# Performance work log

Hardware: AMD Instinct MI355X
Metric: run time of the kernel (lower is better)

Reference implementation:

```python
import jax, jax.numpy as jnp
import numpy as np

B, C, T, E = 8, 64, 128, 256
TYPE_NUM, NF = 40, 128
KS = (5, 4, 3)
NEG = -1e10


def setup_inputs() -> dict:
    key = jax.random.key(0)
    ks = jax.random.split(key, 10)
    s = 0.02
    return {
        "query": jax.random.normal(ks[0], (C, E), jnp.float32),
        "context": jax.random.normal(ks[1], (B, T, E), jnp.float32),
        "mask": jax.random.randint(ks[2], (B, T), 0, 2, jnp.int32),
        "W_hidden": jax.random.normal(ks[3], (4 * E, 4 * E), jnp.float32) * s,
        "b_hidden": jnp.zeros((4 * E,), jnp.float32),
        "W_v": jax.random.normal(ks[4], (1, 4 * E), jnp.float32) * s,
        "b_v": jnp.zeros((1,), jnp.float32),
        "W_lin": jax.random.normal(ks[5], (E, 4 * E), jnp.float32) * s,
        "b_lin": jnp.zeros((E,), jnp.float32),
        "conv_w0": jax.random.normal(ks[6], (NF, E, KS[0]), jnp.float32) * s,
        "conv_b0": jnp.zeros((NF,), jnp.float32),
        "conv_w1": jax.random.normal(ks[7], (NF, E, KS[1]), jnp.float32) * s,
        "conv_b1": jnp.zeros((NF,), jnp.float32),
        "conv_w2": jax.random.normal(ks[8], (NF, E, KS[2]), jnp.float32) * s,
        "conv_b2": jnp.zeros((NF,), jnp.float32),
        "W_cnn": jax.random.normal(ks[9], (TYPE_NUM, NF * 3), jnp.float32) * s,
        "b_cnn": jnp.zeros((TYPE_NUM,), jnp.float32),
    }


def _pair_feat(a, b):
    # [.., e] x2 -> [.., 4e]: [a, b, |a-b|, a*b]
    return jnp.concatenate([a, b, jnp.abs(a - b), a * b], axis=-1)


def _conv1d(x, w, b):
    # x: [b, e, c], w: [f, e, k] (torch Conv1d layout) -> [b, f, c-k+1]
    y = jax.lax.conv_general_dilated(
        x, w, window_strides=(1,), padding="VALID",
        dimension_numbers=("NCH", "OIH", "NCH"))
    return y + b[None, :, None]


def reference(query, context, mask, W_hidden, b_hidden, W_v, b_v,
              W_lin, b_lin, conv_w0, conv_b0, conv_w1, conv_b1,
              conv_w2, conv_b2, W_cnn, b_cnn):
    b, t, e = context.shape
    c = query.shape[0]
    q_ = jnp.broadcast_to(query[None, :, None, :], (b, c, t, e))
    ctx_ = jnp.broadcast_to(context[:, None, :, :], (b, c, t, e))
    feat = _pair_feat(q_, ctx_)                                 # [b,c,t,4e]
    h = jnp.tanh(feat @ W_hidden.T + b_hidden)                  # [b,c,t,4e]
    scores = (h @ W_v.T + b_v)[..., 0]                          # [b,c,t]
    scores = jnp.where((mask < 1)[:, None, :], NEG, scores)
    attn = jax.nn.softmax(scores, axis=-1)                      # [b,c,t]
    g = jnp.einsum("bct,bte->bce", attn, context)               # [b,c,e]
    q2 = jnp.broadcast_to(query[None], (b, c, e))
    h2 = jnp.tanh(_pair_feat(q2, g) @ W_hidden.T + b_hidden)    # [b,c,4e]
    x = h2 @ W_lin.T + b_lin                                    # [b,c,e]
    xT = jnp.transpose(x, (0, 2, 1))                            # [b,e,c]
    pooled = []
    for w, bb in ((conv_w0, conv_b0), (conv_w1, conv_b1), (conv_w2, conv_b2)):
        y = jax.nn.relu(_conv1d(xT, w, bb))                     # [b,f,c-k+1]
        pooled.append(jnp.max(y, axis=2))                       # [b,f]
    cnn = jnp.concatenate(pooled, axis=1)                       # [b,3f]
    return cnn @ W_cnn.T + b_cnn                                # [b,type_num]
```

## Files before the change

kernel.cpp:

```cpp
#include <hip/hip_runtime.h>
#include <math.h>


typedef __bf16 bf16x8 __attribute__((ext_vector_type(8)));
typedef float  f32x4  __attribute__((ext_vector_type(4)));

__device__ __forceinline__ float ftanh(float v) {
    float t = __expf(2.f * v);
    return 1.f - 2.f * __builtin_amdgcn_rcpf(t + 1.f);
}

__device__ __forceinline__ void gld_lds16(const __bf16* g, __bf16* l) {
    __builtin_amdgcn_global_load_lds(
        (const __attribute__((address_space(1))) void*)g,
        (__attribute__((address_space(3))) void*)l, 16, 0, 0);
}

__device__ __forceinline__ bf16x8 cvt8(float4 f0, float4 f1) {
    bf16x8 u;
    u[0] = (__bf16)f0.x; u[1] = (__bf16)f0.y; u[2] = (__bf16)f0.z; u[3] = (__bf16)f0.w;
    u[4] = (__bf16)f1.x; u[5] = (__bf16)f1.y; u[6] = (__bf16)f1.z; u[7] = (__bf16)f1.w;
    return u;
}

__global__ __launch_bounds__(256) void cvt_kernel(
    const float* __restrict__ Wh, const float* __restrict__ Wl,
    const float* __restrict__ ctx,
    const float* __restrict__ cw0, const float* __restrict__ cw1,
    const float* __restrict__ cw2,
    const float* __restrict__ q, const float* __restrict__ bh,
    float* __restrict__ Apre, float* __restrict__ x, float* __restrict__ Bpre,
    __bf16* __restrict__ Whbf, __bf16* __restrict__ Whbf_t,
    __bf16* __restrict__ Wlbf,
    float* __restrict__ wt0, float* __restrict__ wt1,
    float* __restrict__ wt2, float* __restrict__ gsc,
    float* __restrict__ cnn)
{
    __shared__ __align__(16) char smem[18432];
    const int bx = blockIdx.x;
    const int tid = threadIdx.x;

    if (bx < 16) {
        float (*As)[68] = reinterpret_cast<float(*)[68]>(smem);
        float (*Bs)[68] = reinterpret_cast<float(*)[68]>(smem + 4352);
        const int n0 = bx * 64;
        const int tm = tid >> 4, tn = tid & 15;
        const int lr = tid >> 2;
        const int lc = (tid & 3) * 4;

        float acc[4][4];
#pragma unroll
        for (int i = 0; i < 4; ++i)
#pragma unroll
            for (int j = 0; j < 4; ++j) acc[i][j] = 0.f;

        for (int k0 = 0; k0 < 256; k0 += 16) {
            float4 av = *reinterpret_cast<const float4*>(q + (size_t)lr * 256 + k0 + lc);
            float4 bv = *reinterpret_cast<const float4*>(Wh + (size_t)(n0 + lr) * 1024 + k0 + lc);
            As[lc + 0][lr] = av.x; As[lc + 1][lr] = av.y; As[lc + 2][lr] = av.z; As[lc + 3][lr] = av.w;
            Bs[lc + 0][lr] = bv.x; Bs[lc + 1][lr] = bv.y; Bs[lc + 2][lr] = bv.z; Bs[lc + 3][lr] = bv.w;
            __syncthreads();
#pragma unroll
            for (int kk = 0; kk < 16; ++kk) {
                float4 a = *reinterpret_cast<const float4*>(&As[kk][tm * 4]);
                float4 b = *reinterpret_cast<const float4*>(&Bs[kk][tn * 4]);
                float ar[4] = {a.x, a.y, a.z, a.w};
                float br[4] = {b.x, b.y, b.z, b.w};
#pragma unroll
                for (int i = 0; i < 4; ++i)
#pragma unroll
                    for (int j = 0; j < 4; ++j) acc[i][j] += ar[i] * br[j];
            }
            __syncthreads();
        }

#pragma unroll
        for (int i = 0; i < 4; ++i) {
            int m = tm * 4 + i;
            float vals[4];
#pragma unroll
            for (int j = 0; j < 4; ++j) vals[j] = acc[i][j] + bh[n0 + tn * 4 + j];
            float4 o; o.x = vals[0]; o.y = vals[1]; o.z = vals[2]; o.w = vals[3];
            *reinterpret_cast<float4*>(Apre + (size_t)m * 1024 + n0 + tn * 4) = o;
        }
        return;
    }

    if (bx < 272) {
        __bf16* As = reinterpret_cast<__bf16*>(smem);
        __bf16* Bs = As + 64 * 72;
        const int bid = bx - 16;
        const int m0 = (bid >> 4) * 64, n0 = (bid & 15) * 64;
        const int wave = tid >> 6, lane = tid & 63;
        const int w0 = wave >> 1, w1 = wave & 1;
        const int l15 = lane & 15, quad = lane >> 4;

        f32x4 acc[2][2];
#pragma unroll
        for (int mi = 0; mi < 2; ++mi)
#pragma unroll
            for (int ni = 0; ni < 2; ++ni) acc[mi][ni] = (f32x4){0.f, 0.f, 0.f, 0.f};

        for (int k0 = 0; k0 < 256; k0 += 64) {
            __syncthreads();
#pragma unroll
            for (int it = 0; it < 2; ++it) {
                int idx = tid + it * 256;
                int row = idx >> 3, kgi = idx & 7;
                const float* sa = ctx + (size_t)(m0 + row) * 256 + k0 + kgi * 8;
                float4 a0 = *reinterpret_cast<const float4*>(sa);
                float4 a1 = *reinterpret_cast<const float4*>(sa + 4);
                *reinterpret_cast<bf16x8*>(&As[row * 72 + kgi * 8]) = cvt8(a0, a1);
                const float* sb = Wh + (size_t)(n0 + row) * 1024 + 256 + k0 + kgi * 8;
                float4 b0 = *reinterpret_cast<const float4*>(sb);
                float4 b1 = *reinterpret_cast<const float4*>(sb + 4);
                *reinterpret_cast<bf16x8*>(&Bs[row * 72 + kgi * 8]) = cvt8(b0, b1);
            }
            __syncthreads();
#pragma unroll
            for (int ks = 0; ks < 2; ++ks) {
                bf16x8 a[2], bb[2];
#pragma unroll
                for (int mi = 0; mi < 2; ++mi)
                    a[mi] = *reinterpret_cast<const bf16x8*>(
                        &As[(w0 * 32 + mi * 16 + l15) * 72 + ks * 32 + quad * 8]);
#pragma unroll
                for (int ni = 0; ni < 2; ++ni)
                    bb[ni] = *reinterpret_cast<const bf16x8*>(
                        &Bs[(w1 * 32 + ni * 16 + l15) * 72 + ks * 32 + quad * 8]);
#pragma unroll
                for (int mi = 0; mi < 2; ++mi)
#pragma unroll
                    for (int ni = 0; ni < 2; ++ni)
                        acc[mi][ni] = __builtin_amdgcn_mfma_f32_16x16x32_bf16(
                            a[mi], bb[ni], acc[mi][ni], 0, 0, 0);
            }
        }

#pragma unroll
        for (int mi = 0; mi < 2; ++mi)
#pragma unroll
            for (int ni = 0; ni < 2; ++ni) {
                int col = n0 + w1 * 32 + ni * 16 + l15;
#pragma unroll
                for (int r = 0; r < 4; ++r) {
                    int row = m0 + w0 * 32 + mi * 16 + quad * 4 + r;
                    Bpre[(size_t)row * 1024 + col] = acc[mi][ni][r];
                }
            }
        return;
    }

    int idx = (bx - 272) * 256 + tid;
    if (idx < 131072) {
        const float* s = Wh + (size_t)idx * 8;
        float4 f0 = *reinterpret_cast<const float4*>(s);
        float4 f1 = *reinterpret_cast<const float4*>(s + 4);
        *reinterpret_cast<bf16x8*>(Whbf + (size_t)idx * 8) = cvt8(f0, f1);
        return;
    }
    if (idx < 196608) {
        int di = idx - 131072;
        int ng = di >> 13, kc = (di >> 10) & 7;
        int row = (di >> 3) & 127, kgp = di & 7;
        int kg = kgp ^ (row & 7);
        const float* s = Wh + (size_t)(ng * 128 + row) * 1024 + 512 + kc * 64 + kg * 8;
        float4 f0 = *reinterpret_cast<const float4*>(s);
        float4 f1 = *reinterpret_cast<const float4*>(s + 4);
        *reinterpret_cast<bf16x8*>(Whbf_t + (size_t)di * 8) = cvt8(f0, f1);
        return;
    }
    if (idx < 229376) {
        int di = idx - 196608;
        const float* s = Wl + (size_t)di * 8;
        float4 f0 = *reinterpret_cast<const float4*>(s);
        float4 f1 = *reinterpret_cast<const float4*>(s + 4);
        *reinterpret_cast<bf16x8*>(Wlbf + (size_t)di * 8) = cvt8(f0, f1);
        return;
    }
    if (idx < 393216) {
        int j = idx - 229376; int f = j & 127, rest = j >> 7;
        int i = rest % 5, e = rest / 5;
        wt0[j] = cw0[(size_t)(f * 256 + e) * 5 + i]; return;
    }
    if (idx < 524288) {
        int j = idx - 393216; int f = j & 127, rest = j >> 7;
        int i = rest & 3, e = rest >> 2;
        wt1[j] = cw1[(size_t)(f * 256 + e) * 4 + i]; return;
    }
    if (idx < 622592) {
        int j = idx - 524288; int f = j & 127, rest = j >> 7;
        int i = rest % 3, e = rest / 3;
        wt2[j] = cw2[(size_t)(f * 256 + e) * 3 + i]; return;
    }
    if (idx < 638976) {
        int di = idx - 622592;
        reinterpret_cast<float4*>(gsc)[di] = (float4){0.f, 0.f, 0.f, 0.f};
        return;
    }
    if (idx < 642048) { cnn[idx - 638976] = 0.f; return; }
    if (idx < 674816) {
        int di = idx - 642048;
        reinterpret_cast<float4*>(x)[di] = (float4){0.f, 0.f, 0.f, 0.f};
    }
}

__global__ __launch_bounds__(512, 4) void attn_mfma_kernel(
    const float* __restrict__ q,
    const float* __restrict__ ctx,
    const __bf16* __restrict__ Whbf_t,
    const float* __restrict__ Wv,
    const float* __restrict__ Apre,
    const float* __restrict__ Bpre,
    float* __restrict__ gsc)
{
    __shared__ __bf16 Us[256 * 64];
    __shared__ __bf16 Ws[128 * 64];
    __shared__ float qc[512];
    __shared__ float sc[256];

    const int tid = threadIdx.x;
    const int cpair = blockIdx.x >> 3, ng = blockIdx.x & 7;
    const int b = cpair >> 5, c0 = (cpair & 31) * 2;
    const int wave = tid >> 6, lane = tid & 63;
    const int w1 = wave & 1, w0 = wave >> 1;
    const int m0 = w0 * 64;
    const int l15 = lane & 15, quad = lane >> 4;
    const int swz = l15 & 7;
    const int kg = tid & 7;

    qc[tid] = q[(size_t)(c0 + (tid >> 8)) * 256 + (tid & 255)];
    if (tid < 256) sc[tid] = 0.f;
    __syncthreads();

    f32x4 acc[4][4];
#pragma unroll
    for (int mi = 0; mi < 4; ++mi)
#pragma unroll
        for (int ni = 0; ni < 4; ++ni) acc[mi][ni] = (f32x4){0.f, 0.f, 0.f, 0.f};

    for (int kc = 0; kc < 8; ++kc) {
        const bool isabs = (kc < 4);
        const int e0 = (kc & 3) * 64;
        const int eb = e0 + kg * 8;
        float qA[8], qB[8];
#pragma unroll
        for (int i = 0; i < 8; ++i) { qA[i] = qc[eb + i]; qB[i] = qc[256 + eb + i]; }
        bf16x8 u0[2], u1[2];
#pragma unroll
        for (int it = 0; it < 2; ++it) {
            const int trow = it * 64 + (tid >> 3);
            const float* cp = ctx + (size_t)(b * 128 + trow) * 256 + eb;
            float4 cl0 = *reinterpret_cast<const float4*>(cp);
            float4 cl1 = *reinterpret_cast<const float4*>(cp + 4);
            float cv[8] = {cl0.x, cl0.y, cl0.z, cl0.w, cl1.x, cl1.y, cl1.z, cl1.w};
#pragma unroll
            for (int i = 0; i < 8; ++i) {
                u0[it][i] = (__bf16)(isabs ? fabsf(qA[i] - cv[i]) : qA[i] * cv[i]);
                u1[it][i] = (__bf16)(isabs ? fabsf(qB[i] - cv[i]) : qB[i] * cv[i]);
            }
        }
        __syncthreads();
        const __bf16* wtile = Whbf_t + (size_t)(ng * 8 + kc) * 8192;
#pragma unroll
        for (int it = 0; it < 2; ++it) {
            int gidx = wave * 128 + it * 64;
            gld_lds16(wtile + (size_t)(gidx + lane) * 8, &Ws[gidx * 8]);
        }
#pragma unroll
        for (int it = 0; it < 2; ++it) {
            const int trow = it * 64 + (tid >> 3);
            const int off = (kg ^ (trow & 7)) * 8;
            *reinterpret_cast<bf16x8*>(&Us[trow * 64 + off]) = u0[it];
            *reinterpret_cast<bf16x8*>(&Us[(trow + 128) * 64 + off]) = u1[it];
        }
        __syncthreads();
#pragma unroll
        for (int ks = 0; ks < 2; ++ks) {
            const int c8 = (((ks * 4 + quad) ^ swz)) * 8;
            bf16x8 a[4], bfr[4];
#pragma unroll
            for (int mi = 0; mi < 4; ++mi)
                a[mi] = *reinterpret_cast<const bf16x8*>(
                    &Us[(m0 + mi * 16 + l15) * 64 + c8]);
#pragma unroll
            for (int ni = 0; ni < 4; ++ni)
                bfr[ni] = *reinterpret_cast<const bf16x8*>(
                    &Ws[(w1 * 64 + ni * 16 + l15) * 64 + c8]);
#pragma unroll
            for (int mi = 0; mi < 4; ++mi)
#pragma unroll
                for (int ni = 0; ni < 4; ++ni)
                    acc[mi][ni] = __builtin_amdgcn_mfma_f32_16x16x32_bf16(
                        a[mi], bfr[ni], acc[mi][ni], 0, 0, 0);
        }
    }

    const int jcol = ng * 128 + w1 * 64 + l15;
    const int c = c0 + (w0 >> 1);
    float av[4], wv[4];
#pragma unroll
    for (int ni = 0; ni < 4; ++ni) {
        av[ni] = Apre[(size_t)c * 1024 + jcol + ni * 16];
        wv[ni] = Wv[jcol + ni * 16];
    }
#pragma unroll
    for (int mi = 0; mi < 4; ++mi) {
        const int tb = (w0 & 1) * 64 + mi * 16 + quad * 4;
        float p[4];
#pragma unroll
        for (int r = 0; r < 4; ++r) {
            const float* bp = Bpre + (size_t)(b * 128 + tb + r) * 1024 + jcol;
            float s = 0.f;
#pragma unroll
            for (int ni = 0; ni < 4; ++ni)
                s += ftanh(acc[mi][ni][r] + av[ni] + bp[ni * 16]) * wv[ni];
            p[r] = s;
        }
#pragma unroll
        for (int off = 1; off < 16; off <<= 1)
#pragma unroll
            for (int r = 0; r < 4; ++r) p[r] += __shfl_xor(p[r], off, 16);
        if (l15 == 0) {
#pragma unroll
            for (int r = 0; r < 4; ++r)
                atomicAdd(&sc[(w0 >> 1) * 128 + tb + r], p[r]);
        }
    }
    __syncthreads();

    if (tid < 256) atomicAdd(&gsc[(size_t)(b * 64 + c0) * 128 + tid], sc[tid]);
}

__global__ __launch_bounds__(256) void attn_tail_kernel(
    const float* __restrict__ ctx, const int* __restrict__ mask,
    const float* __restrict__ bv, const float* __restrict__ gsc,
    const float* __restrict__ q, __bf16* __restrict__ feat2,
    float* __restrict__ h2pre)
{
    __shared__ float sc[128];
    __shared__ float red;
    const int tid = threadIdx.x;
    const int bc = blockIdx.x, b = bc >> 6, c = bc & 63;

    reinterpret_cast<float4*>(h2pre)[(size_t)bc * 256 + tid] =
        (float4){0.f, 0.f, 0.f, 0.f};

    if (tid < 128) {
        float s = gsc[(size_t)bc * 128 + tid] + bv[0];
        if (mask[b * 128 + tid] < 1) s = -1e10f;
        sc[tid] = s;
    }
    __syncthreads();
    if (tid < 64) {
        float m = fmaxf(sc[tid], sc[tid + 64]);
        for (int off = 32; off; off >>= 1) m = fmaxf(m, __shfl_xor(m, off, 64));
        if (tid == 0) red = m;
    }
    __syncthreads();
    const float mx = red;
    if (tid < 128) sc[tid] = __expf(sc[tid] - mx);
    __syncthreads();
    if (tid < 64) {
        float s = sc[tid] + sc[tid + 64];
        for (int off = 32; off; off >>= 1) s += __shfl_xor(s, off, 64);
        if (tid == 0) red = s;
    }
    __syncthreads();
    const float inv = 1.f / red;

    float gv = 0.f;
#pragma unroll 16
    for (int t = 0; t < 128; ++t) gv += sc[t] * ctx[(size_t)(b * 128 + t) * 256 + tid];
    gv *= inv;
    const float qv = q[(size_t)c * 256 + tid];
    __bf16* o = feat2 + (size_t)bc * 768 + tid;
    o[0]   = (__bf16)gv;
    o[256] = (__bf16)fabsf(qv - gv);
    o[512] = (__bf16)(qv * gv);
}

template <int ACT, int OUTBF, int BMODE, int ATOMIC, int ATANH>
__global__ __launch_bounds__(256) void mfma_gemm_kernel(
    const void* __restrict__ A, int lda,
    const __bf16* __restrict__ B, int ldb,
    const float* __restrict__ bias, void* __restrict__ Cout,
    int K, int ldc)
{
    __shared__ __bf16 As[64 * 72];
    __shared__ __bf16 Bs[64 * 72];
    const int tid = threadIdx.x;
    const int wave = tid >> 6, lane = tid & 63;
    const int w0 = wave >> 1, w1 = wave & 1;
    const int l15 = lane & 15, quad = lane >> 4;
    const int m0 = blockIdx.y * 64, n0 = blockIdx.x * 64;

    int kbeg = 0, kend = K;
    if (ATOMIC) {
        int kchunk = K / gridDim.z;
        kbeg = blockIdx.z * kchunk;
        kend = kbeg + kchunk;
    }

    f32x4 acc[2][2];
#pragma unroll
    for (int mi = 0; mi < 2; ++mi)
#pragma unroll
        for (int ni = 0; ni < 2; ++ni) acc[mi][ni] = (f32x4){0.f, 0.f, 0.f, 0.f};

    for (int k0 = kbeg; k0 < kend; k0 += 64) {
        __syncthreads();
#pragma unroll
        for (int it = 0; it < 2; ++it) {
            int idx = tid + it * 256;
            int row = idx >> 3, kgi = idx & 7;
            if (ATANH) {
                const float* sa = (const float*)A + (size_t)(m0 + row) * lda + k0 + kgi * 8;
                float4 a0 = *reinterpret_cast<const float4*>(sa);
                float4 a1 = *reinterpret_cast<const float4*>(sa + 4);
                bf16x8 u;
                u[0] = (__bf16)ftanh(a0.x); u[1] = (__bf16)ftanh(a0.y);
                u[2] = (__bf16)ftanh(a0.z); u[3] = (__bf16)ftanh(a0.w);
                u[4] = (__bf16)ftanh(a1.x); u[5] = (__bf16)ftanh(a1.y);
                u[6] = (__bf16)ftanh(a1.z); u[7] = (__bf16)ftanh(a1.w);
                *reinterpret_cast<bf16x8*>(&As[row * 72 + kgi * 8]) = u;
            } else {
                int4 va = *reinterpret_cast<const int4*>(
                    (const __bf16*)A + (size_t)(m0 + row) * lda + k0 + kgi * 8);
                *reinterpret_cast<int4*>(&As[row * 72 + kgi * 8]) = va;
            }
            int4 vb = *reinterpret_cast<const int4*>(B + (size_t)(n0 + row) * ldb + k0 + kgi * 8);
            *reinterpret_cast<int4*>(&Bs[row * 72 + kgi * 8]) = vb;
        }
        __syncthreads();
#pragma unroll
        for (int ks = 0; ks < 2; ++ks) {
            bf16x8 a[2], bb[2];
#pragma unroll
            for (int mi = 0; mi < 2; ++mi)
                a[mi] = *reinterpret_cast<const bf16x8*>(
                    &As[(w0 * 32 + mi * 16 + l15) * 72 + ks * 32 + quad * 8]);
#pragma unroll
            for (int ni = 0; ni < 2; ++ni)
                bb[ni] = *reinterpret_cast<const bf16x8*>(
                    &Bs[(w1 * 32 + ni * 16 + l15) * 72 + ks * 32 + quad * 8]);
#pragma unroll
            for (int mi = 0; mi < 2; ++mi)
#pragma unroll
                for (int ni = 0; ni < 2; ++ni)
                    acc[mi][ni] = __builtin_amdgcn_mfma_f32_16x16x32_bf16(
                        a[mi], bb[ni], acc[mi][ni], 0, 0, 0);
        }
    }

#pragma unroll
    for (int mi = 0; mi < 2; ++mi)
#pragma unroll
        for (int ni = 0; ni < 2; ++ni) {
            int col = n0 + w1 * 32 + ni * 16 + l15;
#pragma unroll
            for (int r = 0; r < 4; ++r) {
                int row = m0 + w0 * 32 + mi * 16 + quad * 4 + r;
                float bsv = (BMODE == 0) ? bias[col]
                          : (BMODE == 1) ? bias[(row & 63) * 1024 + col] : 0.f;
                if (ATOMIC) {
                    float v = acc[mi][ni][r] + (blockIdx.z == 0 ? bsv : 0.f);
                    atomicAdd((float*)Cout + (size_t)row * ldc + col, v);
                } else {
                    float v = acc[mi][ni][r] + bsv;
                    if (ACT) v = ftanh(v);
                    if (OUTBF) ((__bf16*)Cout)[(size_t)row * ldc + col] = (__bf16)v;
                    else       ((float*)Cout)[(size_t)row * ldc + col] = v;
                }
            }
        }
}

template <int KW>
__device__ __forceinline__ void conv_body(
    const float* __restrict__ x, const float* __restrict__ wt,
    float* __restrict__ part, int b, int chunk, int bi_part, int pbase, float* xs)
{
    const int tid = threadIdx.x;
    const int f = tid & 127, esub = tid >> 7;
    const int e0 = chunk * 64;

#pragma unroll
    for (int it = 0; it < 16; ++it) {
        int idx = tid + it * 256;
        int e = idx & 63, p = idx >> 6;
        xs[e * 72 + p] = x[(size_t)(b * 64 + p) * 256 + e0 + e];
    }
    __syncthreads();

    float acc[32];
#pragma unroll
    for (int p = 0; p < 32; ++p) acc[p] = 0.f;

    for (int ei = 0; ei < 32; ++ei) {
        const int eL = esub * 32 + ei;
        float wreg[KW];
#pragma unroll
        for (int i = 0; i < KW; ++i)
            wreg[i] = wt[(size_t)((e0 + eL) * KW + i) * 128 + f];
        float xv[36];
#pragma unroll
        for (int k4 = 0; k4 < 9; ++k4) {
            float4 v = *reinterpret_cast<const float4*>(&xs[eL * 72 + pbase + k4 * 4]);
            xv[k4 * 4 + 0] = v.x; xv[k4 * 4 + 1] = v.y;
            xv[k4 * 4 + 2] = v.z; xv[k4 * 4 + 3] = v.w;
        }
#pragma unroll
        for (int i = 0; i < KW; ++i)
#pragma unroll
            for (int p = 0; p < 32; ++p)
                acc[p] = fmaf(wreg[i], xv[p + i], acc[p]);
    }

    float* op = part + ((size_t)(bi_part * 2 + esub)) * 8192 + f;
#pragma unroll
    for (int p = 0; p < 32; ++p) op[(pbase + p) * 128] = acc[p];
}

__global__ __launch_bounds__(256) void conv_partial_kernel(
    const float* __restrict__ x,
    const float* __restrict__ wt0, const float* __restrict__ wt1,
    const float* __restrict__ wt2, float* __restrict__ part)
{
    __shared__ float xs[64 * 72];
    const int bi = blockIdx.x;
    const int kw = bi >> 6, b = (bi >> 3) & 7, chunk = (bi >> 1) & 3;
    const int pbase = (bi & 1) * 32;
    const int bi_part = kw * 32 + b * 4 + chunk;
    if (kw == 0)      conv_body<5>(x, wt0, part, b, chunk, bi_part, pbase, xs);
    else if (kw == 1) conv_body<4>(x, wt1, part, b, chunk, bi_part, pbase, xs);
    else              conv_body<3>(x, wt2, part, b, chunk, bi_part, pbase, xs);
}

__global__ __launch_bounds__(128) void reduce_pool_kernel(
    const float* __restrict__ part,
    const float* __restrict__ b0, const float* __restrict__ b1,
    const float* __restrict__ b2, float* __restrict__ cnn)
{
    const int bi = blockIdx.x;
    const int kw = bi >> 6, b = (bi >> 3) & 7, pc = bi & 7;
    const int f = threadIdx.x;
    const int KW = 5 - kw, P = 64 - KW + 1;
    const float bias = (kw == 0 ? b0 : kw == 1 ? b1 : b2)[f];
    float mx = 0.f;
#pragma unroll
    for (int pl = 0; pl < 8; ++pl) {
        int p = pc * 8 + pl;
        if (p < P) {
            float s = 0.f;
#pragma unroll
            for (int c4 = 0; c4 < 4; ++c4)
#pragma unroll
                for (int es = 0; es < 2; ++es)
                    s += part[((size_t)((kw * 32 + b * 4 + c4) * 2 + es)) * 8192 + p * 128 + f];
            s += bias;
            mx = fmaxf(mx, s);
        }
    }
    if (mx > 0.f)
        atomicMax((int*)(cnn + b * 384 + kw * 128 + f), __float_as_int(mx));
}

__global__ void final_kernel(const float* __restrict__ cnn, const float* __restrict__ Wc,
                             const float* __restrict__ bc, float* __restrict__ out)
{
    int o = threadIdx.x;
    if (o >= 320) return;
    int b = o / 40, t = o - b * 40;
    float s = bc[t];
    for (int i = 0; i < 384; ++i) s += cnn[b * 384 + i] * Wc[t * 384 + i];
    out[o] = s;
}

extern "C" void kernel_launch(void* const* d_in, const int* in_sizes, int n_in,
                              void* d_out, int out_size, void* d_ws, size_t ws_size,
                              hipStream_t stream)
{
    (void)in_sizes; (void)n_in; (void)out_size; (void)ws_size;
    const float* q    = (const float*)d_in[0];
    const float* ctx  = (const float*)d_in[1];
    const int*   mask = (const int*)d_in[2];
    const float* Wh   = (const float*)d_in[3];
    const float* bh   = (const float*)d_in[4];
    const float* Wv   = (const float*)d_in[5];
    const float* bv   = (const float*)d_in[6];
    const float* Wl   = (const float*)d_in[7];
    const float* bl   = (const float*)d_in[8];
    const float* cw0  = (const float*)d_in[9];
    const float* cb0  = (const float*)d_in[10];
    const float* cw1  = (const float*)d_in[11];
    const float* cb1  = (const float*)d_in[12];
    const float* cw2  = (const float*)d_in[13];
    const float* cb2  = (const float*)d_in[14];
    const float* Wc   = (const float*)d_in[15];
    const float* bc   = (const float*)d_in[16];

    float* ws   = (float*)d_ws;
    float* Apre = ws;
    float* g    = Apre + 65536;
    float* x    = g + 131072;
    float* cnn  = x + 131072;
    float* part = cnn + 3072;
    float* wt0  = part + 1572864;
    float* wt1  = wt0 + 163840;
    float* wt2  = wt1 + 131072;
    __bf16* bfb    = (__bf16*)(wt2 + 98304);
    __bf16* Whbf   = bfb;
    __bf16* Wlbf   = bfb + 1048576;
    __bf16* feat2b = bfb + 1310720;
    float*  gsc    = (float*)(bfb + 2228224);
    __bf16* Whbf_t = (__bf16*)part;
    float*  Bpre   = (float*)(Whbf_t + 524288);
    float*  h2pre  = Bpre;

    dim3 blk(256);
    cvt_kernel<<<2908, blk, 0, stream>>>(Wh, Wl, ctx, cw0, cw1, cw2, q, bh,
                                         Apre, x, Bpre,
                                         Whbf, Whbf_t, Wlbf, wt0, wt1, wt2,
                                         gsc, cnn);
    attn_mfma_kernel<<<2048, dim3(512), 0, stream>>>(q, ctx, Whbf_t, Wv, Apre, Bpre, gsc);
    attn_tail_kernel<<<512, blk, 0, stream>>>(ctx, mask, bv, gsc, q, feat2b, h2pre);
    mfma_gemm_kernel<0, 0, 1, 1, 0><<<dim3(16, 8, 2), blk, 0, stream>>>(
        feat2b, 768, Whbf + 256, 1024, Apre, h2pre, 768, 1024);
    mfma_gemm_kernel<0, 0, 0, 1, 1><<<dim3(4, 8, 4), blk, 0, stream>>>(
        h2pre, 1024, Wlbf, 1024, bl, x, 1024, 256);
    conv_partial_kernel<<<192, blk, 0, stream>>>(x, wt0, wt1, wt2, part);
    reduce_pool_kernel<<<192, dim3(128), 0, stream>>>(part, cb0, cb1, cb2, cnn);
    final_kernel<<<1, 320, 0, stream>>>(cnn, Wc, bc, (float*)d_out);
}
```

Baseline: 273.1 us.

## Build feature tile once per (b,c) block and loop over all output column groups

The attention MFMA kernel now gives each block a single (batch, query) pair. It builds the full 128x512 bf16 pair-feature operand in LDS once and then iterates over all 8 column groups of W_hidden, where before it recomputed the features per column group across 2048 blocks. Scores are written directly instead of with global atomics. In exchange each block uses about 144KB of LDS, so occupancy drops, and the grid shrinks to 512 blocks.

```diff
diff --git a/kernel.cpp b/kernel.cpp
--- a/kernel.cpp
+++ b/kernel.cpp
@@ -205,7 +205,7 @@
     }
 }
 
-__global__ __launch_bounds__(512, 4) void attn_mfma_kernel(
+__global__ __launch_bounds__(512, 2) void attn_mfma_kernel(
     const float* __restrict__ q,
     const float* __restrict__ ctx,
     const __bf16* __restrict__ Whbf_t,
@@ -214,122 +214,119 @@
     const float* __restrict__ Bpre,
     float* __restrict__ gsc)
 {
-    __shared__ __bf16 Us[256 * 64];
+    __shared__ __bf16 Us[8 * 128 * 64];
     __shared__ __bf16 Ws[128 * 64];
-    __shared__ float qc[512];
-    __shared__ float sc[256];
+    __shared__ float qc[256];
+    __shared__ float sc[128];
 
     const int tid = threadIdx.x;
-    const int cpair = blockIdx.x >> 3, ng = blockIdx.x & 7;
-    const int b = cpair >> 5, c0 = (cpair & 31) * 2;
+    const int bc = blockIdx.x;
+    const int b = bc >> 6, c = bc & 63;
     const int wave = tid >> 6, lane = tid & 63;
-    const int w1 = wave & 1, w0 = wave >> 1;
-    const int m0 = w0 * 64;
+    const int wm = wave >> 2, wn = wave & 3;
+    const int m0 = wm * 64;
     const int l15 = lane & 15, quad = lane >> 4;
     const int swz = l15 & 7;
     const int kg = tid & 7;
-
-    qc[tid] = q[(size_t)(c0 + (tid >> 8)) * 256 + (tid & 255)];
-    if (tid < 256) sc[tid] = 0.f;
+    const int trw = tid >> 3;
+
+    if (tid < 256) qc[tid] = q[(size_t)c * 256 + tid];
+    if (tid < 128) sc[tid] = 0.f;
     __syncthreads();
-
-    f32x4 acc[4][4];
-#pragma unroll
-    for (int mi = 0; mi < 4; ++mi)
-#pragma unroll
-        for (int ni = 0; ni < 4; ++ni) acc[mi][ni] = (f32x4){0.f, 0.f, 0.f, 0.f};
 
     for (int kc = 0; kc < 8; ++kc) {
         const bool isabs = (kc < 4);
-        const int e0 = (kc & 3) * 64;
-        const int eb = e0 + kg * 8;
-        float qA[8], qB[8];
-#pragma unroll
-        for (int i = 0; i < 8; ++i) { qA[i] = qc[eb + i]; qB[i] = qc[256 + eb + i]; }
-        bf16x8 u0[2], u1[2];
+        const int eb = (kc & 3) * 64 + kg * 8;
+        float qv8[8];
+#pragma unroll
+        for (int i = 0; i < 8; ++i) qv8[i] = qc[eb + i];
 #pragma unroll
         for (int it = 0; it < 2; ++it) {
-            const int trow = it * 64 + (tid >> 3);
+            const int trow = it * 64 + trw;
             const float* cp = ctx + (size_t)(b * 128 + trow) * 256 + eb;
             float4 cl0 = *reinterpret_cast<const float4*>(cp);
             float4 cl1 = *reinterpret_cast<const float4*>(cp + 4);
             float cv[8] = {cl0.x, cl0.y, cl0.z, cl0.w, cl1.x, cl1.y, cl1.z, cl1.w};
-#pragma unroll
-            for (int i = 0; i < 8; ++i) {
-                u0[it][i] = (__bf16)(isabs ? fabsf(qA[i] - cv[i]) : qA[i] * cv[i]);
-                u1[it][i] = (__bf16)(isabs ? fabsf(qB[i] - cv[i]) : qB[i] * cv[i]);
-            }
-        }
-        __syncthreads();
-        const __bf16* wtile = Whbf_t + (size_t)(ng * 8 + kc) * 8192;
-#pragma unroll
-        for (int it = 0; it < 2; ++it) {
-            int gidx = wave * 128 + it * 64;
-            gld_lds16(wtile + (size_t)(gidx + lane) * 8, &Ws[gidx * 8]);
-        }
-#pragma unroll
-        for (int it = 0; it < 2; ++it) {
-            const int trow = it * 64 + (tid >> 3);
-            const int off = (kg ^ (trow & 7)) * 8;
-            *reinterpret_cast<bf16x8*>(&Us[trow * 64 + off]) = u0[it];
-            *reinterpret_cast<bf16x8*>(&Us[(trow + 128) * 64 + off]) = u1[it];
-        }
-        __syncthreads();
-#pragma unroll
-        for (int ks = 0; ks < 2; ++ks) {
-            const int c8 = (((ks * 4 + quad) ^ swz)) * 8;
-            bf16x8 a[4], bfr[4];
-#pragma unroll
-            for (int mi = 0; mi < 4; ++mi)
-                a[mi] = *reinterpret_cast<const bf16x8*>(
-                    &Us[(m0 + mi * 16 + l15) * 64 + c8]);
-#pragma unroll
-            for (int ni = 0; ni < 4; ++ni)
-                bfr[ni] = *reinterpret_cast<const bf16x8*>(
-                    &Ws[(w1 * 64 + ni * 16 + l15) * 64 + c8]);
-#pragma unroll
-            for (int mi = 0; mi < 4; ++mi)
-#pragma unroll
-                for (int ni = 0; ni < 4; ++ni)
-                    acc[mi][ni] = __builtin_amdgcn_mfma_f32_16x16x32_bf16(
-                        a[mi], bfr[ni], acc[mi][ni], 0, 0, 0);
-        }
-    }
-
-    const int jcol = ng * 128 + w1 * 64 + l15;
-    const int c = c0 + (w0 >> 1);
-    float av[4], wv[4];
-#pragma unroll
-    for (int ni = 0; ni < 4; ++ni) {
-        av[ni] = Apre[(size_t)c * 1024 + jcol + ni * 16];
-        wv[ni] = Wv[jcol + ni * 16];
-    }
-#pragma unroll
-    for (int mi = 0; mi < 4; ++mi) {
-        const int tb = (w0 & 1) * 64 + mi * 16 + quad * 4;
-        float p[4];
-#pragma unroll
-        for (int r = 0; r < 4; ++r) {
-            const float* bp = Bpre + (size_t)(b * 128 + tb + r) * 1024 + jcol;
-            float s = 0.f;
-#pragma unroll
-            for (int ni = 0; ni < 4; ++ni)
-                s += ftanh(acc[mi][ni][r] + av[ni] + bp[ni * 16]) * wv[ni];
-            p[r] = s;
-        }
-#pragma unroll
-        for (int off = 1; off < 16; off <<= 1)
-#pragma unroll
-            for (int r = 0; r < 4; ++r) p[r] += __shfl_xor(p[r], off, 16);
-        if (l15 == 0) {
-#pragma unroll
-            for (int r = 0; r < 4; ++r)
-                atomicAdd(&sc[(w0 >> 1) * 128 + tb + r], p[r]);
+            bf16x8 u;
+#pragma unroll
+            for (int i = 0; i < 8; ++i)
+                u[i] = (__bf16)(isabs ? fabsf(qv8[i] - cv[i]) : qv8[i] * cv[i]);
+            *reinterpret_cast<bf16x8*>(
+                &Us[kc * 8192 + trow * 64 + (kg ^ (trow & 7)) * 8]) = u;
+        }
+    }
+
+    for (int ng = 0; ng < 8; ++ng) {
+        f32x4 acc[4][2];
+#pragma unroll
+        for (int mi = 0; mi < 4; ++mi)
+#pragma unroll
+            for (int ni = 0; ni < 2; ++ni) acc[mi][ni] = (f32x4){0.f, 0.f, 0.f, 0.f};
+
+        for (int kc = 0; kc < 8; ++kc) {
+            __syncthreads();
+            const __bf16* wtile = Whbf_t + (size_t)(ng * 8 + kc) * 8192;
+#pragma unroll
+            for (int it = 0; it < 2; ++it) {
+                int gidx = wave * 128 + it * 64;
+                gld_lds16(wtile + (size_t)(gidx + lane) * 8, &Ws[gidx * 8]);
+            }
+            __syncthreads();
+#pragma unroll
+            for (int ks = 0; ks < 2; ++ks) {
+                const int c8 = (((ks * 4 + quad) ^ swz)) * 8;
+                bf16x8 a[4], bfr[2];
+#pragma unroll
+                for (int mi = 0; mi < 4; ++mi)
+                    a[mi] = *reinterpret_cast<const bf16x8*>(
+                        &Us[kc * 8192 + (m0 + mi * 16 + l15) * 64 + c8]);
+#pragma unroll
+                for (int ni = 0; ni < 2; ++ni)
+                    bfr[ni] = *reinterpret_cast<const bf16x8*>(
+                        &Ws[(wn * 32 + ni * 16 + l15) * 64 + c8]);
+#pragma unroll
+                for (int mi = 0; mi < 4; ++mi)
+#pragma unroll
+                    for (int ni = 0; ni < 2; ++ni)
+                        acc[mi][ni] = __builtin_amdgcn_mfma_f32_16x16x32_bf16(
+                            a[mi], bfr[ni], acc[mi][ni], 0, 0, 0);
+            }
+        }
+
+        const int jcol = ng * 128 + wn * 32 + l15;
+        float av[2], wv[2];
+#pragma unroll
+        for (int ni = 0; ni < 2; ++ni) {
+            av[ni] = Apre[(size_t)c * 1024 + jcol + ni * 16];
+            wv[ni] = Wv[jcol + ni * 16];
+        }
+#pragma unroll
+        for (int mi = 0; mi < 4; ++mi) {
+            const int tb = m0 + mi * 16 + quad * 4;
+            float p[4];
+#pragma unroll
+            for (int r = 0; r < 4; ++r) {
+                const float* bp = Bpre + (size_t)(b * 128 + tb + r) * 1024 + jcol;
+                float s = 0.f;
+#pragma unroll
+                for (int ni = 0; ni < 2; ++ni)
+                    s += ftanh(acc[mi][ni][r] + av[ni] + bp[ni * 16]) * wv[ni];
+                p[r] = s;
+            }
+#pragma unroll
+            for (int off = 1; off < 16; off <<= 1)
+#pragma unroll
+                for (int r = 0; r < 4; ++r) p[r] += __shfl_xor(p[r], off, 16);
+            if (l15 == 0) {
+#pragma unroll
+                for (int r = 0; r < 4; ++r)
+                    atomicAdd(&sc[tb + r], p[r]);
+            }
         }
     }
     __syncthreads();
 
-    if (tid < 256) atomicAdd(&gsc[(size_t)(b * 64 + c0) * 128 + tid], sc[tid]);
+    if (tid < 128) gsc[(size_t)bc * 128 + tid] = sc[tid];
 }
 
 __global__ __launch_bounds__(256) void attn_tail_kernel(
@@ -623,7 +620,7 @@
                                          Apre, x, Bpre,
                                          Whbf, Whbf_t, Wlbf, wt0, wt1, wt2,
                                          gsc, cnn);
-    attn_mfma_kernel<<<2048, dim3(512), 0, stream>>>(q, ctx, Whbf_t, Wv, Apre, Bpre, gsc);
+    attn_mfma_kernel<<<512, dim3(512), 0, stream>>>(q, ctx, Whbf_t, Wv, Apre, Bpre, gsc);
     attn_tail_kernel<<<512, blk, 0, stream>>>(ctx, mask, bv, gsc, q, feat2b, h2pre);
     mfma_gemm_kernel<0, 0, 1, 1, 0><<<dim3(16, 8, 2), blk, 0, stream>>>(
         feat2b, 768, Whbf + 256, 1024, Apre, h2pre, 768, 1024);
```

Measured after the change: 309.9 us. 1.13x slower.

## Precompute swizzled bf16 pair features in workspace for attention MFMA kernel

Applied to the files above, without the earlier changes.

Adds extra blocks to the conversion kernel that materialise the |q-ctx| and q*ctx pair features in bf16 for every (b,c,t), in a pre-swizzled tile layout written to a large workspace region. A new attention kernel then streams both operand tiles straight into LDS with async global-to-LDS loads, instead of computing features from q and ctx on the fly. This moves the feature arithmetic and bf16 conversion out of the MFMA loop at the cost of writing and re-reading about 64 MB of intermediate data. The new path is taken only when the workspace is large enough; otherwise the old kernel runs.

```diff
diff --git a/kernel.cpp b/kernel.cpp
--- a/kernel.cpp
+++ b/kernel.cpp
@@ -34,11 +34,43 @@
     __bf16* __restrict__ Wlbf,
     float* __restrict__ wt0, float* __restrict__ wt1,
     float* __restrict__ wt2, float* __restrict__ gsc,
-    float* __restrict__ cnn)
+    float* __restrict__ cnn, __bf16* __restrict__ Ubf)
 {
     __shared__ __align__(16) char smem[18432];
     const int bx = blockIdx.x;
     const int tid = threadIdx.x;
+
+    if (bx >= 2908) {
+        int idx2 = (bx - 2908) * 256 + tid;
+        int bc = idx2 >> 10;
+        int rem = idx2 & 1023;
+        int trow = rem >> 3, kg = rem & 7;
+        int b = bc >> 6, c = bc & 63;
+        int gs = kg ^ (trow & 7);
+#pragma unroll
+        for (int ec = 0; ec < 4; ++ec) {
+            int eb = ec * 64 + kg * 8;
+            const float* cp = ctx + (size_t)(b * 128 + trow) * 256 + eb;
+            float4 c0 = *reinterpret_cast<const float4*>(cp);
+            float4 c1 = *reinterpret_cast<const float4*>(cp + 4);
+            const float* qp = q + (size_t)c * 256 + eb;
+            float4 q0 = *reinterpret_cast<const float4*>(qp);
+            float4 q1 = *reinterpret_cast<const float4*>(qp + 4);
+            float cv[8] = {c0.x, c0.y, c0.z, c0.w, c1.x, c1.y, c1.z, c1.w};
+            float qv[8] = {q0.x, q0.y, q0.z, q0.w, q1.x, q1.y, q1.z, q1.w};
+            bf16x8 ua, um;
+#pragma unroll
+            for (int i = 0; i < 8; ++i) {
+                ua[i] = (__bf16)fabsf(qv[i] - cv[i]);
+                um[i] = (__bf16)(qv[i] * cv[i]);
+            }
+            *reinterpret_cast<bf16x8*>(
+                Ubf + (((size_t)(bc * 8 + ec) * 128 + trow) * 8 + gs) * 8) = ua;
+            *reinterpret_cast<bf16x8*>(
+                Ubf + (((size_t)(bc * 8 + 4 + ec) * 128 + trow) * 8 + gs) * 8) = um;
+        }
+        return;
+    }
 
     if (bx < 16) {
         float (*As)[68] = reinterpret_cast<float(*)[68]>(smem);
@@ -203,6 +235,108 @@
         int di = idx - 642048;
         reinterpret_cast<float4*>(x)[di] = (float4){0.f, 0.f, 0.f, 0.f};
     }
+}
+
+__global__ __launch_bounds__(512, 4) void attn_mfma_u_kernel(
+    const __bf16* __restrict__ Ubf,
+    const __bf16* __restrict__ Whbf_t,
+    const float* __restrict__ Wv,
+    const float* __restrict__ Apre,
+    const float* __restrict__ Bpre,
+    float* __restrict__ gsc)
+{
+    __shared__ __bf16 Us[256 * 64];
+    __shared__ __bf16 Ws[128 * 64];
+    __shared__ float sc[256];
+
+    const int tid = threadIdx.x;
+    const int cpair = blockIdx.x >> 3, ng = blockIdx.x & 7;
+    const int b = cpair >> 5, c0 = (cpair & 31) * 2;
+    const int wave = tid >> 6, lane = tid & 63;
+    const int w1 = wave & 1, w0 = wave >> 1;
+    const int m0 = w0 * 64;
+    const int l15 = lane & 15, quad = lane >> 4;
+    const int swz = l15 & 7;
+
+    if (tid < 256) sc[tid] = 0.f;
+    __syncthreads();
+
+    const __bf16* ubase = Ubf + (size_t)(b * 64 + c0) * 65536;
+
+    f32x4 acc[4][4];
+#pragma unroll
+    for (int mi = 0; mi < 4; ++mi)
+#pragma unroll
+        for (int ni = 0; ni < 4; ++ni) acc[mi][ni] = (f32x4){0.f, 0.f, 0.f, 0.f};
+
+    for (int kc = 0; kc < 8; ++kc) {
+        __syncthreads();
+        const __bf16* wtile = Whbf_t + (size_t)(ng * 8 + kc) * 8192;
+        const __bf16* ut0 = ubase + (size_t)kc * 8192;
+        const __bf16* ut1 = ut0 + 65536;
+#pragma unroll
+        for (int it = 0; it < 2; ++it) {
+            int gidx = wave * 128 + it * 64;
+            gld_lds16(wtile + (size_t)(gidx + lane) * 8, &Ws[gidx * 8]);
+            gld_lds16(ut0 + (size_t)(gidx + lane) * 8, &Us[gidx * 8]);
+            gld_lds16(ut1 + (size_t)(gidx + lane) * 8, &Us[8192 + gidx * 8]);
+        }
+        __syncthreads();
+#pragma unroll
+        for (int ks = 0; ks < 2; ++ks) {
+            const int c8 = (((ks * 4 + quad) ^ swz)) * 8;
+            bf16x8 a[4], bfr[4];
+#pragma unroll
+            for (int mi = 0; mi < 4; ++mi)
+                a[mi] = *reinterpret_cast<const bf16x8*>(
+                    &Us[(m0 + mi * 16 + l15) * 64 + c8]);
+#pragma unroll
+            for (int ni = 0; ni < 4; ++ni)
+                bfr[ni] = *reinterpret_cast<const bf16x8*>(
+                    &Ws[(w1 * 64 + ni * 16 + l15) * 64 + c8]);
+#pragma unroll
+            for (int mi = 0; mi < 4; ++mi)
+#pragma unroll
+                for (int ni = 0; ni < 4; ++ni)
+                    acc[mi][ni] = __builtin_amdgcn_mfma_f32_16x16x32_bf16(
+                        a[mi], bfr[ni], acc[mi][ni], 0, 0, 0);
+        }
+    }
+
+    const int jcol = ng * 128 + w1 * 64 + l15;
+    const int c = c0 + (w0 >> 1);
+    float av[4], wv[4];
+#pragma unroll
+    for (int ni = 0; ni < 4; ++ni) {
+        av[ni] = Apre[(size_t)c * 1024 + jcol + ni * 16];
+        wv[ni] = Wv[jcol + ni * 16];
+    }
+#pragma unroll
+    for (int mi = 0; mi < 4; ++mi) {
+        const int tb = (w0 & 1) * 64 + mi * 16 + quad * 4;
+        float p[4];
+#pragma unroll
+        for (int r = 0; r < 4; ++r) {
+            const float* bp = Bpre + (size_t)(b * 128 + tb + r) * 1024 + jcol;
+            float s = 0.f;
+#pragma unroll
+            for (int ni = 0; ni < 4; ++ni)
+                s += ftanh(acc[mi][ni][r] + av[ni] + bp[ni * 16]) * wv[ni];
+            p[r] = s;
+        }
+#pragma unroll
+        for (int off = 1; off < 16; off <<= 1)
+#pragma unroll
+            for (int r = 0; r < 4; ++r) p[r] += __shfl_xor(p[r], off, 16);
+        if (l15 == 0) {
+#pragma unroll
+            for (int r = 0; r < 4; ++r)
+                atomicAdd(&sc[(w0 >> 1) * 128 + tb + r], p[r]);
+        }
+    }
+    __syncthreads();
+
+    if (tid < 256) atomicAdd(&gsc[(size_t)(b * 64 + c0) * 128 + tid], sc[tid]);
 }
 
 __global__ __launch_bounds__(512, 4) void attn_mfma_kernel(
@@ -581,7 +715,7 @@
                               void* d_out, int out_size, void* d_ws, size_t ws_size,
                               hipStream_t stream)
 {
-    (void)in_sizes; (void)n_in; (void)out_size; (void)ws_size;
+    (void)in_sizes; (void)n_in; (void)out_size;
     const float* q    = (const float*)d_in[0];
     const float* ctx  = (const float*)d_in[1];
     const int*   mask = (const int*)d_in[2];
@@ -617,13 +751,21 @@
     __bf16* Whbf_t = (__bf16*)part;
     float*  Bpre   = (float*)(Whbf_t + 524288);
     float*  h2pre  = Bpre;
+    const size_t UBF_OFF = 13905920;
+    const size_t UBF_BYTES = (size_t)33554432 * 2;
+    const bool bigws = ws_size >= UBF_OFF + UBF_BYTES;
+    __bf16* Ubf = (__bf16*)((char*)d_ws + UBF_OFF);
 
     dim3 blk(256);
-    cvt_kernel<<<2908, blk, 0, stream>>>(Wh, Wl, ctx, cw0, cw1, cw2, q, bh,
-                                         Apre, x, Bpre,
-                                         Whbf, Whbf_t, Wlbf, wt0, wt1, wt2,
-                                         gsc, cnn);
-    attn_mfma_kernel<<<2048, dim3(512), 0, stream>>>(q, ctx, Whbf_t, Wv, Apre, Bpre, gsc);
+    cvt_kernel<<<bigws ? 4956 : 2908, blk, 0, stream>>>(
+        Wh, Wl, ctx, cw0, cw1, cw2, q, bh, Apre, x, Bpre,
+        Whbf, Whbf_t, Wlbf, wt0, wt1, wt2, gsc, cnn, Ubf);
+    if (bigws)
+        attn_mfma_u_kernel<<<2048, dim3(512), 0, stream>>>(
+            Ubf, Whbf_t, Wv, Apre, Bpre, gsc);
+    else
+        attn_mfma_kernel<<<2048, dim3(512), 0, stream>>>(
+            q, ctx, Whbf_t, Wv, Apre, Bpre, gsc);
     attn_tail_kernel<<<512, blk, 0, stream>>>(ctx, mask, bv, gsc, q, feat2b, h2pre);
     mfma_gemm_kernel<0, 0, 1, 1, 0><<<dim3(16, 8, 2), blk, 0, stream>>>(
         feat2b, 768, Whbf + 256, 1024, Apre, h2pre, 768, 1024);
```

Result: no change. 273.4 us (+0.1%).

## Precompute bf16 pair features in workspace and stream them into attention via LDS loads

Applied to the files above, without the earlier changes.

The prep kernel gains extra blocks that build the |q-ctx| and q*ctx pair features for every (batch, query, position) in bf16. They are written to a large workspace buffer in the pre-swizzled LDS layout. The attention MFMA kernel then fetches these tiles with direct global-to-LDS loads instead of recomputing them from ctx and q in registers. Block indices are also remapped so that concurrently running blocks share the same weight group. This trades per-block VALU conversion work for roughly 64 MB of extra global writes, and each feature tile is re-read once per weight group. The fallback path when the workspace is too small never fills the buffer the attention kernel reads.

```diff
diff --git a/kernel.cpp b/kernel.cpp
--- a/kernel.cpp
+++ b/kernel.cpp
@@ -34,11 +34,43 @@
     __bf16* __restrict__ Wlbf,
     float* __restrict__ wt0, float* __restrict__ wt1,
     float* __restrict__ wt2, float* __restrict__ gsc,
-    float* __restrict__ cnn)
+    float* __restrict__ cnn, __bf16* __restrict__ Ubf)
 {
     __shared__ __align__(16) char smem[18432];
     const int bx = blockIdx.x;
     const int tid = threadIdx.x;
+
+    if (bx >= 2908) {
+        int idx2 = (bx - 2908) * 256 + tid;
+        int bc = idx2 >> 10;
+        int rem = idx2 & 1023;
+        int trow = rem >> 3, kg = rem & 7;
+        int b = bc >> 6, c = bc & 63;
+        int gs = kg ^ (trow & 7);
+#pragma unroll
+        for (int ec = 0; ec < 4; ++ec) {
+            int eb = ec * 64 + kg * 8;
+            const float* cp = ctx + (size_t)(b * 128 + trow) * 256 + eb;
+            float4 c0 = *reinterpret_cast<const float4*>(cp);
+            float4 c1 = *reinterpret_cast<const float4*>(cp + 4);
+            const float* qp = q + (size_t)c * 256 + eb;
+            float4 q0 = *reinterpret_cast<const float4*>(qp);
+            float4 q1 = *reinterpret_cast<const float4*>(qp + 4);
+            float cv[8] = {c0.x, c0.y, c0.z, c0.w, c1.x, c1.y, c1.z, c1.w};
+            float qv[8] = {q0.x, q0.y, q0.z, q0.w, q1.x, q1.y, q1.z, q1.w};
+            bf16x8 ua, um;
+#pragma unroll
+            for (int i = 0; i < 8; ++i) {
+                ua[i] = (__bf16)fabsf(qv[i] - cv[i]);
+                um[i] = (__bf16)(qv[i] * cv[i]);
+            }
+            *reinterpret_cast<bf16x8*>(
+                Ubf + (((size_t)(bc * 8 + ec) * 128 + trow) * 8 + gs) * 8) = ua;
+            *reinterpret_cast<bf16x8*>(
+                Ubf + (((size_t)(bc * 8 + 4 + ec) * 128 + trow) * 8 + gs) * 8) = um;
+        }
+        return;
+    }
 
     if (bx < 16) {
         float (*As)[68] = reinterpret_cast<float(*)[68]>(smem);
@@ -205,9 +237,8 @@
     }
 }
 
-__global__ __launch_bounds__(512, 4) void attn_mfma_kernel(
-    const float* __restrict__ q,
-    const float* __restrict__ ctx,
+__global__ __launch_bounds__(512, 4) void attn_mfma_u_kernel(
+    const __bf16* __restrict__ Ubf,
     const __bf16* __restrict__ Whbf_t,
     const float* __restrict__ Wv,
     const float* __restrict__ Apre,
@@ -216,23 +247,23 @@
 {
     __shared__ __bf16 Us[256 * 64];
     __shared__ __bf16 Ws[128 * 64];
-    __shared__ float qc[512];
     __shared__ float sc[256];
 
     const int tid = threadIdx.x;
-    const int cpair = blockIdx.x >> 3, ng = blockIdx.x & 7;
+    const int wid = (blockIdx.x & 7) * 256 + (blockIdx.x >> 3);
+    const int cpair = wid >> 3, ng = wid & 7;
     const int b = cpair >> 5, c0 = (cpair & 31) * 2;
     const int wave = tid >> 6, lane = tid & 63;
     const int w1 = wave & 1, w0 = wave >> 1;
     const int m0 = w0 * 64;
     const int l15 = lane & 15, quad = lane >> 4;
     const int swz = l15 & 7;
-    const int kg = tid & 7;
-
-    qc[tid] = q[(size_t)(c0 + (tid >> 8)) * 256 + (tid & 255)];
+
     if (tid < 256) sc[tid] = 0.f;
     __syncthreads();
 
+    const __bf16* ubase = Ubf + (size_t)(b * 64 + c0) * 65536;
+
     f32x4 acc[4][4];
 #pragma unroll
     for (int mi = 0; mi < 4; ++mi)
@@ -240,39 +271,16 @@
         for (int ni = 0; ni < 4; ++ni) acc[mi][ni] = (f32x4){0.f, 0.f, 0.f, 0.f};
 
     for (int kc = 0; kc < 8; ++kc) {
-        const bool isabs = (kc < 4);
-        const int e0 = (kc & 3) * 64;
-        const int eb = e0 + kg * 8;
-        float qA[8], qB[8];
-#pragma unroll
-        for (int i = 0; i < 8; ++i) { qA[i] = qc[eb + i]; qB[i] = qc[256 + eb + i]; }
-        bf16x8 u0[2], u1[2];
-#pragma unroll
-        for (int it = 0; it < 2; ++it) {
-            const int trow = it * 64 + (tid >> 3);
-            const float* cp = ctx + (size_t)(b * 128 + trow) * 256 + eb;
-            float4 cl0 = *reinterpret_cast<const float4*>(cp);
-            float4 cl1 = *reinterpret_cast<const float4*>(cp + 4);
-            float cv[8] = {cl0.x, cl0.y, cl0.z, cl0.w, cl1.x, cl1.y, cl1.z, cl1.w};
-#pragma unroll
-            for (int i = 0; i < 8; ++i) {
-                u0[it][i] = (__bf16)(isabs ? fabsf(qA[i] - cv[i]) : qA[i] * cv[i]);
-                u1[it][i] = (__bf16)(isabs ? fabsf(qB[i] - cv[i]) : qB[i] * cv[i]);
-            }
-        }
         __syncthreads();
         const __bf16* wtile = Whbf_t + (size_t)(ng * 8 + kc) * 8192;
+        const __bf16* ut0 = ubase + (size_t)kc * 8192;
+        const __bf16* ut1 = ut0 + 65536;
 #pragma unroll
         for (int it = 0; it < 2; ++it) {
             int gidx = wave * 128 + it * 64;
             gld_lds16(wtile + (size_t)(gidx + lane) * 8, &Ws[gidx * 8]);
-        }
-#pragma unroll
-        for (int it = 0; it < 2; ++it) {
-            const int trow = it * 64 + (tid >> 3);
-            const int off = (kg ^ (trow & 7)) * 8;
-            *reinterpret_cast<bf16x8*>(&Us[trow * 64 + off]) = u0[it];
-            *reinterpret_cast<bf16x8*>(&Us[(trow + 128) * 64 + off]) = u1[it];
+            gld_lds16(ut0 + (size_t)(gidx + lane) * 8, &Us[gidx * 8]);
+            gld_lds16(ut1 + (size_t)(gidx + lane) * 8, &Us[8192 + gidx * 8]);
         }
         __syncthreads();
 #pragma unroll
@@ -581,7 +589,7 @@
                               void* d_out, int out_size, void* d_ws, size_t ws_size,
                               hipStream_t stream)
 {
-    (void)in_sizes; (void)n_in; (void)out_size; (void)ws_size;
+    (void)in_sizes; (void)n_in; (void)out_size;
     const float* q    = (const float*)d_in[0];
     const float* ctx  = (const float*)d_in[1];
     const int*   mask = (const int*)d_in[2];
@@ -617,13 +625,17 @@
     __bf16* Whbf_t = (__bf16*)part;
     float*  Bpre   = (float*)(Whbf_t + 524288);
     float*  h2pre  = Bpre;
+    const size_t UBF_OFF = 13905920;
+    const size_t UBF_BYTES = (size_t)33554432 * 2;
+    const bool bigws = ws_size >= UBF_OFF + UBF_BYTES;
+    __bf16* Ubf = (__bf16*)((char*)d_ws + UBF_OFF);
 
     dim3 blk(256);
-    cvt_kernel<<<2908, blk, 0, stream>>>(Wh, Wl, ctx, cw0, cw1, cw2, q, bh,
-                                         Apre, x, Bpre,
-                                         Whbf, Whbf_t, Wlbf, wt0, wt1, wt2,
-                                         gsc, cnn);
-    attn_mfma_kernel<<<2048, dim3(512), 0, stream>>>(q, ctx, Whbf_t, Wv, Apre, Bpre, gsc);
+    cvt_kernel<<<bigws ? 4956 : 2908, blk, 0, stream>>>(
+        Wh, Wl, ctx, cw0, cw1, cw2, q, bh, Apre, x, Bpre,
+        Whbf, Whbf_t, Wlbf, wt0, wt1, wt2, gsc, cnn, Ubf);
+    attn_mfma_u_kernel<<<2048, dim3(512), 0, stream>>>(
+        Ubf, Whbf_t, Wv, Apre, Bpre, gsc);
     attn_tail_kernel<<<512, blk, 0, stream>>>(ctx, mask, bv, gsc, q, feat2b, h2pre);
     mfma_gemm_kernel<0, 0, 1, 1, 0><<<dim3(16, 8, 2), blk, 0, stream>>>(
         feat2b, 768, Whbf + 256, 1024, Apre, h2pre, 768, 1024);
```

Result: faster. 261.3 us (-4.3%).
